# Optimization experiments

Hardware: AMD Instinct MI355X
Metric: run time of the kernel (lower is better)

The kernel has to match this reference:

```python
import jax, jax.numpy as jnp
import numpy as np

B, T, D, H = 4, 2048, 1024, 16
HS = D // H  # 64
EPS = 1e-5


def layer_norm(x, g, b):
    mu = jnp.mean(x, axis=-1, keepdims=True)
    var = jnp.mean(jnp.square(x - mu), axis=-1, keepdims=True)
    return (x - mu) * jax.lax.rsqrt(var + EPS) * g + b


def setup_inputs() -> dict:
    key = jax.random.key(0)
    ks = jax.random.split(key, 12)
    s_in = 1.0 / np.sqrt(D)
    s_proj = 1.0 / np.sqrt(H * HS)
    s_ff = 1.0 / np.sqrt(4 * D)
    return {
        "x": jax.random.normal(ks[0], (B, T, D), jnp.float32),
        "ln1_g": jnp.ones((D,), jnp.float32),
        "ln1_b": jnp.zeros((D,), jnp.float32),
        # per-head Q/K/V weights stacked: [H, D, HS] (x @ W, no bias)
        "wq": jax.random.uniform(ks[1], (H, D, HS), jnp.float32, -s_in, s_in),
        "wk": jax.random.uniform(ks[2], (H, D, HS), jnp.float32, -s_in, s_in),
        "wv": jax.random.uniform(ks[3], (H, D, HS), jnp.float32, -s_in, s_in),
        "w_proj": jax.random.uniform(ks[4], (H * HS, D), jnp.float32, -s_proj, s_proj),
        "b_proj": jax.random.uniform(ks[5], (D,), jnp.float32, -s_proj, s_proj),
        "ln2_g": jnp.ones((D,), jnp.float32),
        "ln2_b": jnp.zeros((D,), jnp.float32),
        "w1": jax.random.uniform(ks[6], (D, 4 * D), jnp.float32, -s_in, s_in),
        "b1": jax.random.uniform(ks[7], (4 * D,), jnp.float32, -s_in, s_in),
        "w2": jax.random.uniform(ks[8], (4 * D, D), jnp.float32, -s_ff, s_ff),
        "b2": jax.random.uniform(ks[9], (D,), jnp.float32, -s_ff, s_ff),
    }


def reference(x, ln1_g, ln1_b, wq, wk, wv, w_proj, b_proj, ln2_g, ln2_b, w1, b1, w2, b2):
    # --- pre-LN self-attention ---
    xn = layer_norm(x, ln1_g, ln1_b)
    q = jnp.einsum("btd,hdk->bhtk", xn, wq)
    k = jnp.einsum("btd,hdk->bhtk", xn, wk)
    v = jnp.einsum("btd,hdk->bhtk", xn, wv)
    scale = HS ** -0.5
    scores = jnp.einsum("bhtk,bhsk->bhts", q, k) * scale  # [B,H,T,T]
    t = x.shape[1]
    causal = jnp.tril(jnp.ones((t, t), bool))
    scores = jnp.where(causal, scores, -jnp.inf)
    attn = jax.nn.softmax(scores, axis=-1)  # dropout p=0 -> identity
    ctx = jnp.einsum("bhts,bhsk->bhtk", attn, v)
    ctx = jnp.transpose(ctx, (0, 2, 1, 3)).reshape(x.shape[0], t, H * HS)
    x = x + ctx @ w_proj + b_proj
    # --- pre-LN feed-forward ---
    xn = layer_norm(x, ln2_g, ln2_b)
    h = jax.nn.relu(xn @ w1 + b1)
    return x + h @ w2 + b2
```

## Files before the change

kernel.cpp:

```cpp
#include <hip/hip_runtime.h>

typedef __bf16 bf16;
typedef __attribute__((ext_vector_type(8))) __bf16 bf16x8;
typedef __attribute__((ext_vector_type(4))) __bf16 bf16x4;
typedef __attribute__((ext_vector_type(4))) float f32x4;

static constexpr int Bc = 4, Tc = 2048, Dc = 1024, Hc = 16, HSc = 64, DFF = 4096;
static constexpr int Mrows = Bc * Tc;

#define DEV __device__ __forceinline__

DEV void load_lds16(const void* g, void* l) {
  __builtin_amdgcn_global_load_lds(
      (const __attribute__((address_space(1))) void*)g,
      (__attribute__((address_space(3))) void*)l, 16, 0, 0);
}

__global__ void repack_qkv_kernel(const float* __restrict__ wq,
                                  const float* __restrict__ wk,
                                  const float* __restrict__ wv,
                                  bf16* __restrict__ dst) {
  __shared__ float tile[64][65];
  const int dblk = blockIdx.x;
  const int z = blockIdx.y;
  const int w = z >> 4, h = z & 15;
  const float* src = (w == 0 ? wq : (w == 1 ? wk : wv)) + (size_t)h * Dc * HSc;
  const int tx = threadIdx.x, ty = threadIdx.y;
#pragma unroll
  for (int i = 0; i < 16; ++i)
    tile[ty + i * 4][tx] = src[(size_t)(dblk * 64 + ty + i * 4) * HSc + tx];
  __syncthreads();
#pragma unroll
  for (int i = 0; i < 16; ++i) {
    const int s = ty + i * 4;
    dst[((size_t)w * 1024 + h * 64 + s) * Dc + dblk * 64 + tx] = (bf16)tile[tx][s];
  }
}

__global__ void transpose_to_bf16_kernel(const float* __restrict__ src,
                                         bf16* __restrict__ dst, int R, int C) {
  __shared__ float tile[64][65];
  const int r0 = blockIdx.x * 64, c0 = blockIdx.y * 64;
  const int tx = threadIdx.x, ty = threadIdx.y;
#pragma unroll
  for (int i = 0; i < 16; ++i)
    tile[ty + i * 4][tx] = src[(size_t)(r0 + ty + i * 4) * C + c0 + tx];
  __syncthreads();
#pragma unroll
  for (int i = 0; i < 16; ++i)
    dst[(size_t)(c0 + ty + i * 4) * R + r0 + tx] = (bf16)tile[tx][ty + i * 4];
}

__global__ __launch_bounds__(256) void ln_kernel(const float* __restrict__ x,
                                                 const float* __restrict__ gam,
                                                 const float* __restrict__ bet,
                                                 bf16* __restrict__ out) {
  const int row = blockIdx.x;
  const int t = threadIdx.x;
  const float4 v = ((const float4*)(x + (size_t)row * Dc))[t];
  float s = v.x + v.y + v.z + v.w;
  float s2 = v.x * v.x + v.y * v.y + v.z * v.z + v.w * v.w;
#pragma unroll
  for (int m = 1; m < 64; m <<= 1) {
    s += __shfl_xor(s, m);
    s2 += __shfl_xor(s2, m);
  }
  __shared__ float red[8];
  const int wid = t >> 6;
  if ((t & 63) == 0) { red[wid * 2] = s; red[wid * 2 + 1] = s2; }
  __syncthreads();
  s = red[0] + red[2] + red[4] + red[6];
  s2 = red[1] + red[3] + red[5] + red[7];
  const float mean = s * (1.f / Dc);
  const float var = s2 * (1.f / Dc) - mean * mean;
  const float rstd = rsqrtf(var + 1e-5f);
  const float4 gv = ((const float4*)gam)[t];
  const float4 bv = ((const float4*)bet)[t];
  bf16x4 o;
  o[0] = (bf16)((v.x - mean) * rstd * gv.x + bv.x);
  o[1] = (bf16)((v.y - mean) * rstd * gv.y + bv.y);
  o[2] = (bf16)((v.z - mean) * rstd * gv.z + bv.z);
  o[3] = (bf16)((v.w - mean) * rstd * gv.w + bv.w);
  *(bf16x4*)(out + (size_t)row * Dc + t * 4) = o;
}

template <int MODE, int KTOT, int NSTRIDE>
__global__ __launch_bounds__(256, 2) void gemm_kernel(
    const bf16* __restrict__ A, const bf16* __restrict__ BT,
    const float* __restrict__ bias, const float* __restrict__ resid,
    float* __restrict__ outf, bf16* __restrict__ outb,
    bf16* __restrict__ qo, bf16* __restrict__ ko, bf16* __restrict__ vto) {
  __shared__ __attribute__((aligned(16))) bf16 As[128 * 32];
  __shared__ __attribute__((aligned(16))) bf16 Bs[128 * 32];
  const int tid = threadIdx.x;
  const int wid = tid >> 6, lane = tid & 63;
  const int g = lane >> 4, c = lane & 15;
  const int wr = wid >> 1, wc = wid & 1;
  const int bm = blockIdx.x, bn = blockIdx.y;

  f32x4 acc[4][4];
#pragma unroll
  for (int i = 0; i < 4; ++i)
#pragma unroll
    for (int j = 0; j < 4; ++j)
#pragma unroll
      for (int r = 0; r < 4; ++r) acc[i][j][r] = 0.f;

  const bf16* gA = A + (size_t)(bm * 128 + wid * 32 + (lane >> 2)) * KTOT + (lane & 3) * 8;
  const bf16* gB = BT + (size_t)(bn * 128 + wid * 32 + (lane >> 2)) * KTOT + (lane & 3) * 8;
  bf16* lA0 = &As[(wid * 32) * 32];
  bf16* lA1 = &As[(wid * 32 + 16) * 32];
  bf16* lB0 = &Bs[(wid * 32) * 32];
  bf16* lB1 = &Bs[(wid * 32 + 16) * 32];

  for (int kt = 0; kt < KTOT / 32; ++kt) {
    load_lds16(gA, lA0);
    load_lds16(gA + (size_t)16 * KTOT, lA1);
    load_lds16(gB, lB0);
    load_lds16(gB + (size_t)16 * KTOT, lB1);
    gA += 32;
    gB += 32;
    __syncthreads();
    bf16x8 af[4], bfr[4];
#pragma unroll
    for (int mi = 0; mi < 4; ++mi)
      af[mi] = *(const bf16x8*)&As[(wr * 64 + mi * 16 + c) * 32 + g * 8];
#pragma unroll
    for (int ni = 0; ni < 4; ++ni)
      bfr[ni] = *(const bf16x8*)&Bs[(wc * 64 + ni * 16 + c) * 32 + g * 8];
#pragma unroll
    for (int mi = 0; mi < 4; ++mi)
#pragma unroll
      for (int ni = 0; ni < 4; ++ni)
        acc[mi][ni] =
            __builtin_amdgcn_mfma_f32_16x16x32_bf16(af[mi], bfr[ni], acc[mi][ni], 0, 0, 0);
    __syncthreads();
  }

#pragma unroll
  for (int ni = 0; ni < 4; ++ni) {
    const int n = bn * 128 + wc * 64 + ni * 16 + c;
    float bi = 0.f;
    if (MODE != 0) bi = bias[n];
#pragma unroll
    for (int mi = 0; mi < 4; ++mi) {
      const int m0 = bm * 128 + wr * 64 + mi * 16 + g * 4;
      if (MODE == 0) {
        const int w = n >> 10, n1 = n & 1023, h = n1 >> 6, sidx = n1 & 63;
        const int b = m0 >> 11, t0 = m0 & 2047;
        if (w == 0) {
#pragma unroll
          for (int r = 0; r < 4; ++r)
            qo[(size_t)(b * Hc + h) * (Tc * HSc) + (size_t)(t0 + r) * HSc + sidx] =
                (bf16)(acc[mi][ni][r] * 0.125f);
        } else if (w == 1) {
#pragma unroll
          for (int r = 0; r < 4; ++r)
            ko[(size_t)(b * Hc + h) * (Tc * HSc) + (size_t)(t0 + r) * HSc + sidx] =
                (bf16)acc[mi][ni][r];
        } else {
          bf16x4 pk;
#pragma unroll
          for (int r = 0; r < 4; ++r) pk[r] = (bf16)acc[mi][ni][r];
          *(bf16x4*)&vto[((size_t)(b * Hc + h) * HSc + sidx) * Tc + t0] = pk;
        }
      } else if (MODE == 1 || MODE == 3) {
#pragma unroll
        for (int r = 0; r < 4; ++r) {
          const size_t idx = (size_t)(m0 + r) * NSTRIDE + n;
          outf[idx] = acc[mi][ni][r] + bi + resid[idx];
        }
      } else {
#pragma unroll
        for (int r = 0; r < 4; ++r)
          outb[(size_t)(m0 + r) * NSTRIDE + n] = (bf16)fmaxf(acc[mi][ni][r] + bi, 0.f);
      }
    }
  }
}

__global__ __launch_bounds__(256, 2) void attn_kernel(const bf16* __restrict__ q,
                                                      const bf16* __restrict__ k,
                                                      const bf16* __restrict__ vt,
                                                      bf16* __restrict__ ctx) {
  __shared__ __attribute__((aligned(16))) bf16 Kl[2][4096];
  __shared__ __attribute__((aligned(16))) bf16 Vl[2][4096];
  __shared__ __attribute__((aligned(16))) bf16 P[4][32][72];
  const int d0 = blockIdx.x;
  const int L = (d0 & 7) * 64 + (d0 >> 3);
  const int bh = L >> 3, p = L & 7;
  const int tid = threadIdx.x;
  const int wid = tid >> 6, lane = tid & 63;
  const int g = lane >> 4, c = lane & 15;
  const bf16* qh = q + (size_t)bh * Tc * HSc;
  const char* kh = (const char*)(k + (size_t)bh * Tc * HSc);
  const char* vh = (const char*)(vt + (size_t)bh * HSc * Tc);
  const int b = bh >> 4, h = bh & 15;

  const int sw = ((lane >> 3) & 7) << 4;
  const int soK = (lane * 16) ^ sw;
  const int vrow = lane >> 3;
  const int vcol = ((lane & 7) * 16) ^ sw;
  const int rsw = (c & 7) << 4;

  for (int g2 = 0; g2 < 2; ++g2) {
    const int grp = g2 ? p : 15 - p;
    const int ktB = 2 * grp + 1;
    const int ktW = 2 * grp + (wid >> 1);
    const int row0 = grp * 128 + wid * 32;
    const bf16* qb = qh + (size_t)row0 * HSc;

    bf16x8 qf[2][2];
#pragma unroll
    for (int mi = 0; mi < 2; ++mi)
#pragma unroll
      for (int kk = 0; kk < 2; ++kk)
        qf[mi][kk] = *(const bf16x8*)&qb[(size_t)(mi * 16 + c) * HSc + kk * 32 + g * 8];

    f32x4 o[2][4];
    float m_[2][4], ls[2][4];
#pragma unroll
    for (int mi = 0; mi < 2; ++mi)
#pragma unroll
      for (int r = 0; r < 4; ++r) {
        m_[mi][r] = -1e30f;
        ls[mi][r] = 0.f;
#pragma unroll
        for (int di = 0; di < 4; ++di) o[mi][di][r] = 0.f;
      }

    auto stage = [&](int buf, int kt) {
      const char* kb = kh + (size_t)kt * 8192;
      const char* vb = vh + (size_t)kt * 128;
#pragma unroll
      for (int i = 0; i < 4; ++i) {
        const int idx = wid * 4 + i;
        if (idx < 8) {
          load_lds16(kb + idx * 1024 + soK, (char*)&Kl[buf][0] + idx * 1024);
        } else {
          const int j = idx - 8;
          load_lds16(vb + (size_t)(j * 8 + vrow) * (Tc * 2) + vcol,
                     (char*)&Vl[buf][0] + j * 1024);
        }
      }
    };

    stage(0, 0);
    __syncthreads();
    int cur = 0;
    for (int kt = 0; kt <= ktB; ++kt) {
      if (kt < ktB) stage(cur ^ 1, kt + 1);
      if (kt <= ktW) {
        const char* Kb = (const char*)&Kl[cur][0];
        bf16x8 kf[4][2];
#pragma unroll
        for (int ni = 0; ni < 4; ++ni)
#pragma unroll
          for (int kk = 0; kk < 2; ++kk)
            kf[ni][kk] = *(const bf16x8*)(Kb + (ni * 16 + c) * 128 +
                                          (((kk << 6) | (g << 4)) ^ rsw));
        f32x4 s[2][4];
#pragma unroll
        for (int mi = 0; mi < 2; ++mi)
#pragma unroll
          for (int ni = 0; ni < 4; ++ni)
#pragma unroll
            for (int r = 0; r < 4; ++r) s[mi][ni][r] = 0.f;
        __builtin_amdgcn_s_setprio(1);
#pragma unroll
        for (int kk = 0; kk < 2; ++kk)
#pragma unroll
          for (int mi = 0; mi < 2; ++mi)
#pragma unroll
            for (int ni = 0; ni < 4; ++ni)
              s[mi][ni] = __builtin_amdgcn_mfma_f32_16x16x32_bf16(qf[mi][kk], kf[ni][kk],
                                                                  s[mi][ni], 0, 0, 0);
        __builtin_amdgcn_s_setprio(0);

        if (kt == ktW) {
#pragma unroll
          for (int mi = 0; mi < 2; ++mi)
#pragma unroll
            for (int ni = 0; ni < 4; ++ni)
#pragma unroll
              for (int r = 0; r < 4; ++r) {
                const int row = row0 + mi * 16 + g * 4 + r;
                const int col = kt * 64 + ni * 16 + c;
                if (col > row) s[mi][ni][r] = -1e30f;
              }
        }

        float pm[2][4];
        int need = 0;
#pragma unroll
        for (int mi = 0; mi < 2; ++mi)
#pragma unroll
          for (int r = 0; r < 4; ++r) {
            pm[mi][r] =
                fmaxf(fmaxf(s[mi][0][r], s[mi][1][r]), fmaxf(s[mi][2][r], s[mi][3][r]));
            need |= (pm[mi][r] > m_[mi][r] + 8.f) ? 1 : 0;
          }
        if (__any(need)) {
#pragma unroll
          for (int mi = 0; mi < 2; ++mi)
#pragma unroll
            for (int r = 0; r < 4; ++r) {
              float mx = pm[mi][r];
#pragma unroll
              for (int msk = 1; msk < 16; msk <<= 1) mx = fmaxf(mx, __shfl_xor(mx, msk));
              const float mn = fmaxf(m_[mi][r], mx);
              const float al = __expf(m_[mi][r] - mn);
              m_[mi][r] = mn;
              ls[mi][r] *= al;
#pragma unroll
              for (int di = 0; di < 4; ++di) o[mi][di][r] *= al;
            }
        }
#pragma unroll
        for (int mi = 0; mi < 2; ++mi)
#pragma unroll
          for (int r = 0; r < 4; ++r) {
            float ps = 0.f;
#pragma unroll
            for (int ni = 0; ni < 4; ++ni) {
              const float pv = __expf(s[mi][ni][r] - m_[mi][r]);
              ps += pv;
              P[wid][mi * 16 + g * 4 + r][ni * 16 + c] = (bf16)pv;
            }
            ls[mi][r] += ps;
          }
        asm volatile("s_waitcnt lgkmcnt(0)" ::: "memory");
        __builtin_amdgcn_sched_barrier(0);

        bf16x8 pf[2][2];
#pragma unroll
        for (int mi = 0; mi < 2; ++mi)
#pragma unroll
          for (int kk = 0; kk < 2; ++kk)
            pf[mi][kk] = *(const bf16x8*)&P[wid][mi * 16 + c][kk * 32 + g * 8];
        const char* Vb = (const char*)&Vl[cur][0];
#pragma unroll
        for (int di = 0; di < 4; ++di) {
          bf16x8 vf0 = *(const bf16x8*)(Vb + (di * 16 + c) * 128 + ((g << 4) ^ rsw));
          bf16x8 vf1 =
              *(const bf16x8*)(Vb + (di * 16 + c) * 128 + (((1 << 6) | (g << 4)) ^ rsw));
          __builtin_amdgcn_s_setprio(1);
#pragma unroll
          for (int mi = 0; mi < 2; ++mi) {
            o[mi][di] = __builtin_amdgcn_mfma_f32_16x16x32_bf16(pf[mi][0], vf0, o[mi][di], 0, 0, 0);
            o[mi][di] = __builtin_amdgcn_mfma_f32_16x16x32_bf16(pf[mi][1], vf1, o[mi][di], 0, 0, 0);
          }
          __builtin_amdgcn_s_setprio(0);
        }
      }
      __syncthreads();
      cur ^= 1;
    }

#pragma unroll
    for (int mi = 0; mi < 2; ++mi)
#pragma unroll
      for (int r = 0; r < 4; ++r) {
        float l = ls[mi][r];
#pragma unroll
        for (int msk = 1; msk < 16; msk <<= 1) l += __shfl_xor(l, msk);
        const float inv = 1.f / l;
        const int t = row0 + mi * 16 + g * 4 + r;
#pragma unroll
        for (int di = 0; di < 4; ++di)
          ctx[((size_t)(b * Tc + t)) * Dc + h * 64 + di * 16 + c] =
              (bf16)(o[mi][di][r] * inv);
      }
  }
}

extern "C" void kernel_launch(void* const* d_in, const int* in_sizes, int n_in,
                              void* d_out, int out_size, void* d_ws, size_t ws_size,
                              hipStream_t stream) {
  (void)in_sizes; (void)n_in; (void)out_size; (void)ws_size;
  const float* x      = (const float*)d_in[0];
  const float* ln1_g  = (const float*)d_in[1];
  const float* ln1_b  = (const float*)d_in[2];
  const float* wq     = (const float*)d_in[3];
  const float* wk     = (const float*)d_in[4];
  const float* wv     = (const float*)d_in[5];
  const float* w_proj = (const float*)d_in[6];
  const float* b_proj = (const float*)d_in[7];
  const float* ln2_g  = (const float*)d_in[8];
  const float* ln2_b  = (const float*)d_in[9];
  const float* w1     = (const float*)d_in[10];
  const float* b1     = (const float*)d_in[11];
  const float* w2     = (const float*)d_in[12];
  const float* b2     = (const float*)d_in[13];
  float* out = (float*)d_out;
  char* ws = (char*)d_ws;

  bf16* qbuf   = (bf16*)(ws + 0);
  bf16* kbuf   = (bf16*)(ws + 16777216);
  bf16* vtbuf  = (bf16*)(ws + 33554432);
  bf16* ctxbuf = (bf16*)(ws + 50331648);
  bf16* wqkvT  = (bf16*)(ws + 67108864);
  bf16* hbuf   = (bf16*)(ws + 0);
  bf16* wprojT = (bf16*)(ws + 73400320);
  bf16* w1T    = (bf16*)(ws + 75497472);
  bf16* w2T    = (bf16*)(ws + 83886080);
  bf16* xn     = (bf16*)(ws + 92274688);
  float* x1buf = (float*)(ws + 109051904);

  repack_qkv_kernel<<<dim3(16, 48), dim3(64, 4), 0, stream>>>(wq, wk, wv, wqkvT);
  transpose_to_bf16_kernel<<<dim3(16, 16), dim3(64, 4), 0, stream>>>(w_proj, wprojT, 1024, 1024);
  transpose_to_bf16_kernel<<<dim3(16, 64), dim3(64, 4), 0, stream>>>(w1, w1T, 1024, 4096);
  transpose_to_bf16_kernel<<<dim3(64, 16), dim3(64, 4), 0, stream>>>(w2, w2T, 4096, 1024);

  ln_kernel<<<Mrows, 256, 0, stream>>>(x, ln1_g, ln1_b, xn);
  gemm_kernel<0, 1024, 0><<<dim3(64, 24), 256, 0, stream>>>(
      xn, wqkvT, nullptr, nullptr, nullptr, nullptr, qbuf, kbuf, vtbuf);
  attn_kernel<<<512, 256, 0, stream>>>(qbuf, kbuf, vtbuf, ctxbuf);
  gemm_kernel<1, 1024, 1024><<<dim3(64, 8), 256, 0, stream>>>(
      ctxbuf, wprojT, b_proj, x, x1buf, nullptr, nullptr, nullptr, nullptr);
  ln_kernel<<<Mrows, 256, 0, stream>>>(x1buf, ln2_g, ln2_b, xn);
  gemm_kernel<2, 1024, 4096><<<dim3(64, 32), 256, 0, stream>>>(
      xn, w1T, b1, nullptr, nullptr, hbuf, nullptr, nullptr, nullptr);
  gemm_kernel<3, 4096, 1024><<<dim3(64, 8), 256, 0, stream>>>(
      hbuf, w2T, b2, x1buf, out, nullptr, nullptr, nullptr, nullptr);
}
```

Before: 392.2 us.

## Replace GEMM with 8-wave double-buffered swizzled-LDS kernel and larger tiles

Replaces the 128x128x32 single-buffer GEMM with a 512-thread kernel using 256xBN tiles, K-step 64, double-buffered LDS filled by direct global-to-LDS loads for the next tile while MFMAs run on the current one. It adds XOR-swizzled LDS addressing to avoid bank conflicts, grouped block remapping for L2 locality, and s_setprio around the MFMA bursts. The aim is to hide memory latency and raise arithmetic intensity. The cost is one block per CU, more LDS and registers, and fewer blocks for the N=1024 GEMMs (256 blocks), which may leave CUs idle.

After: 471.7 us. 1.2x slower.

```diff
diff --git a/kernel.cpp b/kernel.cpp
--- a/kernel.cpp
+++ b/kernel.cpp
@@ -84,96 +84,151 @@
   *(bf16x4*)(out + (size_t)row * Dc + t * 4) = o;
 }
 
-template <int MODE, int KTOT, int NSTRIDE>
-__global__ __launch_bounds__(256, 2) void gemm_kernel(
+template <int MODE, int KTOT, int BN>
+__global__ __launch_bounds__(512, 1) void gemm8_kernel(
     const bf16* __restrict__ A, const bf16* __restrict__ BT,
     const float* __restrict__ bias, const float* __restrict__ resid,
     float* __restrict__ outf, bf16* __restrict__ outb,
     bf16* __restrict__ qo, bf16* __restrict__ ko, bf16* __restrict__ vto) {
-  __shared__ __attribute__((aligned(16))) bf16 As[128 * 32];
-  __shared__ __attribute__((aligned(16))) bf16 Bs[128 * 32];
+  constexpr int NF = BN / 64;
+  constexpr int NSPAN = BN / 4;
+  constexpr int NT = KTOT / 64;
+  constexpr int HT = 2 + BN / 128;
+  constexpr int NSTR = (MODE == 2) ? 4096 : 1024;
+
+  __shared__ __attribute__((aligned(16))) bf16 As[2][2][128 * 64];
+  __shared__ __attribute__((aligned(16))) bf16 Bs[2][BN / 128][128 * 64];
+
   const int tid = threadIdx.x;
   const int wid = tid >> 6, lane = tid & 63;
-  const int g = lane >> 4, c = lane & 15;
-  const int wr = wid >> 1, wc = wid & 1;
-  const int bm = blockIdx.x, bn = blockIdx.y;
-
-  f32x4 acc[4][4];
-#pragma unroll
-  for (int i = 0; i < 4; ++i)
-#pragma unroll
-    for (int j = 0; j < 4; ++j)
+  const int g = (lane >> 4) & 3, c = lane & 15;
+  const int wm = wid >> 2, wn = wid & 3;
+
+  const int gx = gridDim.x;
+  const int total = gx * gridDim.y;
+  const int flat = blockIdx.y * gx + blockIdx.x;
+  const int q8 = total >> 3;
+  const int sz = (flat & 7) * q8 + (flat >> 3);
+  const int bm = sz % gx, bn = sz / gx;
+
+  f32x4 acc[8][NF];
+#pragma unroll
+  for (int i = 0; i < 8; ++i)
+#pragma unroll
+    for (int j = 0; j < NF; ++j)
 #pragma unroll
       for (int r = 0; r < 4; ++r) acc[i][j][r] = 0.f;
 
-  const bf16* gA = A + (size_t)(bm * 128 + wid * 32 + (lane >> 2)) * KTOT + (lane & 3) * 8;
-  const bf16* gB = BT + (size_t)(bn * 128 + wid * 32 + (lane >> 2)) * KTOT + (lane & 3) * 8;
-  bf16* lA0 = &As[(wid * 32) * 32];
-  bf16* lA1 = &As[(wid * 32 + 16) * 32];
-  bf16* lB0 = &Bs[(wid * 32) * 32];
-  bf16* lB1 = &Bs[(wid * 32 + 16) * 32];
-
-  for (int kt = 0; kt < KTOT / 32; ++kt) {
-    load_lds16(gA, lA0);
-    load_lds16(gA + (size_t)16 * KTOT, lA1);
-    load_lds16(gB, lB0);
-    load_lds16(gB + (size_t)16 * KTOT, lB1);
-    gA += 32;
-    gB += 32;
-    __syncthreads();
-    bf16x8 af[4], bfr[4];
-#pragma unroll
-    for (int mi = 0; mi < 4; ++mi)
-      af[mi] = *(const bf16x8*)&As[(wr * 64 + mi * 16 + c) * 32 + g * 8];
-#pragma unroll
-    for (int ni = 0; ni < 4; ++ni)
-      bfr[ni] = *(const bf16x8*)&Bs[(wc * 64 + ni * 16 + c) * 32 + g * 8];
-#pragma unroll
-    for (int mi = 0; mi < 4; ++mi)
-#pragma unroll
-      for (int ni = 0; ni < 4; ++ni)
-        acc[mi][ni] =
-            __builtin_amdgcn_mfma_f32_16x16x32_bf16(af[mi], bfr[ni], acc[mi][ni], 0, 0, 0);
-    __syncthreads();
+  const int swz = ((lane >> 3) & 7) << 4;
+  const int scol = ((lane & 7) << 4) ^ swz;
+  const int srow_lo = lane >> 3;
+  const char* Agl = (const char*)A;
+  const char* Bgl = (const char*)BT;
+  const int arow0 = bm * 256;
+  const int brow0 = bn * BN;
+
+  auto stage = [&](int buf, int kt, int ht) {
+#pragma unroll
+    for (int j = 0; j < 2; ++j) {
+      const int ci = j * 8 + wid;
+      const int r = ci * 8 + srow_lo;
+      if (ht < 2) {
+        load_lds16(Agl + ((size_t)(arow0 + ht * 128 + r) * KTOT + kt * 64) * 2 + scol,
+                   (char*)&As[buf][ht][0] + ci * 1024);
+      } else {
+        load_lds16(Bgl + ((size_t)(brow0 + (ht - 2) * 128 + r) * KTOT + kt * 64) * 2 + scol,
+                   (char*)&Bs[buf][ht - 2][0] + ci * 1024);
+      }
+    }
+  };
+
+#pragma unroll
+  for (int h = 0; h < HT; ++h) stage(0, 0, h);
+
+  for (int t = 0; t < NT; ++t) {
+    const int b = t & 1;
+    const char* Ab = (const char*)&As[b][wm][0];
+    const char* Bb0 = (const char*)&Bs[b][0][0];
+    bf16x8 bfr[NF];
+#pragma unroll
+    for (int p = 0; p < 4; ++p) {
+      const int mh = p & 1, ks = p >> 1;
+      if (p == 0) {
+        __builtin_amdgcn_s_barrier();
+        if (t + 1 < NT) {
+          stage(b ^ 1, t + 1, 0);
+          asm volatile("s_waitcnt vmcnt(2)" ::: "memory");
+        } else {
+          asm volatile("s_waitcnt vmcnt(0)" ::: "memory");
+        }
+        __builtin_amdgcn_s_barrier();
+        __builtin_amdgcn_sched_barrier(0);
+      } else {
+        if (t + 1 < NT && p < HT) stage(b ^ 1, t + 1, p);
+      }
+      if ((p & 1) == 0) {
+#pragma unroll
+        for (int nf = 0; nf < NF; ++nf) {
+          const int ncol = wn * NSPAN + nf * 16 + c;
+          const char* Bb = Bb0 + (size_t)(ncol >> 7) * (128 * 64 * 2);
+          const int lr = ncol & 127;
+          bfr[nf] = *(const bf16x8*)(Bb + lr * 128 + ((ks * 64 + g * 16) ^ ((c & 7) << 4)));
+        }
+      }
+      bf16x8 af[4];
+#pragma unroll
+      for (int i = 0; i < 4; ++i) {
+        const int lr = (mh * 4 + i) * 16 + c;
+        af[i] = *(const bf16x8*)(Ab + lr * 128 + ((ks * 64 + g * 16) ^ ((c & 7) << 4)));
+      }
+      __builtin_amdgcn_s_setprio(1);
+#pragma unroll
+      for (int i = 0; i < 4; ++i)
+#pragma unroll
+        for (int nf = 0; nf < NF; ++nf)
+          acc[mh * 4 + i][nf] = __builtin_amdgcn_mfma_f32_16x16x32_bf16(
+              af[i], bfr[nf], acc[mh * 4 + i][nf], 0, 0, 0);
+      __builtin_amdgcn_s_setprio(0);
+    }
   }
 
 #pragma unroll
-  for (int ni = 0; ni < 4; ++ni) {
-    const int n = bn * 128 + wc * 64 + ni * 16 + c;
+  for (int nf = 0; nf < NF; ++nf) {
+    const int n = bn * BN + wn * NSPAN + nf * 16 + c;
     float bi = 0.f;
     if (MODE != 0) bi = bias[n];
 #pragma unroll
-    for (int mi = 0; mi < 4; ++mi) {
-      const int m0 = bm * 128 + wr * 64 + mi * 16 + g * 4;
+    for (int fr = 0; fr < 8; ++fr) {
+      const int m0 = bm * 256 + wm * 128 + fr * 16 + g * 4;
       if (MODE == 0) {
         const int w = n >> 10, n1 = n & 1023, h = n1 >> 6, sidx = n1 & 63;
-        const int b = m0 >> 11, t0 = m0 & 2047;
+        const int b2 = m0 >> 11, t0 = m0 & 2047;
         if (w == 0) {
 #pragma unroll
           for (int r = 0; r < 4; ++r)
-            qo[(size_t)(b * Hc + h) * (Tc * HSc) + (size_t)(t0 + r) * HSc + sidx] =
-                (bf16)(acc[mi][ni][r] * 0.125f);
+            qo[(size_t)(b2 * Hc + h) * (Tc * HSc) + (size_t)(t0 + r) * HSc + sidx] =
+                (bf16)(acc[fr][nf][r] * 0.125f);
         } else if (w == 1) {
 #pragma unroll
           for (int r = 0; r < 4; ++r)
-            ko[(size_t)(b * Hc + h) * (Tc * HSc) + (size_t)(t0 + r) * HSc + sidx] =
-                (bf16)acc[mi][ni][r];
+            ko[(size_t)(b2 * Hc + h) * (Tc * HSc) + (size_t)(t0 + r) * HSc + sidx] =
+                (bf16)acc[fr][nf][r];
         } else {
           bf16x4 pk;
 #pragma unroll
-          for (int r = 0; r < 4; ++r) pk[r] = (bf16)acc[mi][ni][r];
-          *(bf16x4*)&vto[((size_t)(b * Hc + h) * HSc + sidx) * Tc + t0] = pk;
+          for (int r = 0; r < 4; ++r) pk[r] = (bf16)acc[fr][nf][r];
+          *(bf16x4*)&vto[((size_t)(b2 * Hc + h) * HSc + sidx) * Tc + t0] = pk;
         }
       } else if (MODE == 1 || MODE == 3) {
 #pragma unroll
         for (int r = 0; r < 4; ++r) {
-          const size_t idx = (size_t)(m0 + r) * NSTRIDE + n;
-          outf[idx] = acc[mi][ni][r] + bi + resid[idx];
+          const size_t idx = (size_t)(m0 + r) * NSTR + n;
+          outf[idx] = acc[fr][nf][r] + bi + resid[idx];
         }
       } else {
 #pragma unroll
         for (int r = 0; r < 4; ++r)
-          outb[(size_t)(m0 + r) * NSTRIDE + n] = (bf16)fmaxf(acc[mi][ni][r] + bi, 0.f);
+          outb[(size_t)(m0 + r) * NSTR + n] = (bf16)fmaxf(acc[fr][nf][r] + bi, 0.f);
       }
     }
   }
@@ -413,14 +468,14 @@
   transpose_to_bf16_kernel<<<dim3(64, 16), dim3(64, 4), 0, stream>>>(w2, w2T, 4096, 1024);
 
   ln_kernel<<<Mrows, 256, 0, stream>>>(x, ln1_g, ln1_b, xn);
-  gemm_kernel<0, 1024, 0><<<dim3(64, 24), 256, 0, stream>>>(
+  gemm8_kernel<0, 1024, 256><<<dim3(32, 12), 512, 0, stream>>>(
       xn, wqkvT, nullptr, nullptr, nullptr, nullptr, qbuf, kbuf, vtbuf);
   attn_kernel<<<512, 256, 0, stream>>>(qbuf, kbuf, vtbuf, ctxbuf);
-  gemm_kernel<1, 1024, 1024><<<dim3(64, 8), 256, 0, stream>>>(
+  gemm8_kernel<1, 1024, 128><<<dim3(32, 8), 512, 0, stream>>>(
       ctxbuf, wprojT, b_proj, x, x1buf, nullptr, nullptr, nullptr, nullptr);
   ln_kernel<<<Mrows, 256, 0, stream>>>(x1buf, ln2_g, ln2_b, xn);
-  gemm_kernel<2, 1024, 4096><<<dim3(64, 32), 256, 0, stream>>>(
+  gemm8_kernel<2, 1024, 256><<<dim3(32, 16), 512, 0, stream>>>(
       xn, w1T, b1, nullptr, nullptr, hbuf, nullptr, nullptr, nullptr);
-  gemm_kernel<3, 4096, 1024><<<dim3(64, 8), 256, 0, stream>>>(
+  gemm8_kernel<3, 4096, 128><<<dim3(32, 8), 512, 0, stream>>>(
       hbuf, w2T, b2, x1buf, out, nullptr, nullptr, nullptr, nullptr);
 }
```
